# Kernel optimization log

Hardware: AMD Instinct MI355X
Metric: run time of the kernel (lower is better)

The kernel has to match this reference:

```python
import jax, jax.numpy as jnp
import numpy as np

NUM_EMBEDDINGS = 1024
EMBEDDING_DIM = 256
COMMITMENT_COST = 0.25
B, C, T = 16, 256, 4096


def setup_inputs() -> dict:
    key = jax.random.key(0)
    k_in, k_cb = jax.random.split(key)
    inputs = jax.random.normal(k_in, (B, C, T), dtype=jnp.float32)
    # matches nn.Embedding init uniform_(-1/K, 1/K)
    codebook = jax.random.uniform(
        k_cb, (NUM_EMBEDDINGS, EMBEDDING_DIM), dtype=jnp.float32,
        minval=-1.0 / NUM_EMBEDDINGS, maxval=1.0 / NUM_EMBEDDINGS)
    return {"inputs": inputs, "codebook": codebook}


def reference(inputs, codebook):
    # inputs: [B, C, T] -> [B, T, C] (channel-last), eval mode (no dead-code swap)
    x = jnp.transpose(inputs, (0, 2, 1))            # [B, T, C]
    flat = x.reshape(-1, EMBEDDING_DIM)             # [N, D]
    distances = (jnp.sum(flat * flat, axis=1, keepdims=True)
                 + jnp.sum(codebook * codebook, axis=1)
                 - 2.0 * jnp.matmul(flat, codebook.T))   # [N, K]
    encoding_indices = jnp.argmin(distances, axis=1)     # [N]
    quantized = codebook[encoding_indices].reshape(x.shape)  # [B, T, C]
    sg = jax.lax.stop_gradient
    e_latent_loss = jnp.mean(jnp.square(sg(quantized) - x))
    q_latent_loss = jnp.mean(jnp.square(quantized - sg(x)))
    vq_loss = e_latent_loss + COMMITMENT_COST * q_latent_loss
    quantized_st = x + sg(quantized - x)                 # straight-through
    quantized_st = jnp.transpose(quantized_st, (0, 2, 1))  # back to [B, C, T]
    indices = encoding_indices.reshape(B, T)
    return quantized_st, vq_loss, indices
```

## Files before the change

kernel.cpp:

```cpp
#include <hip/hip_runtime.h>
#include <stdint.h>

#define DIMS 256
#define NT 4096
#define NROWS 65536
#define THETA 1.5e-4f

typedef float    f32x4_t __attribute__((ext_vector_type(4)));
typedef _Float16 f16x8_t __attribute__((ext_vector_type(8)));
typedef _Float16 f16x4_t __attribute__((ext_vector_type(4)));

__global__ __launch_bounds__(64) void vq_prep(const float* __restrict__ cb,
                                              float* __restrict__ se,
                                              _Float16* __restrict__ cb16){
  __shared__ float sq[256];
  const int k = blockIdx.x;
  const int tid = threadIdx.x;
  float4 v = *(const float4*)(cb + (size_t)k*256 + tid*4);
  f16x4_t p;
  p.x = (_Float16)(v.x * 512.f);
  p.y = (_Float16)(v.y * 512.f);
  p.z = (_Float16)(v.z * 512.f);
  p.w = (_Float16)(v.w * 512.f);
  *(f16x4_t*)(cb16 + (size_t)k*256 + tid*4) = p;
  sq[tid*4+0] = __fmul_rn(v.x, v.x);
  sq[tid*4+1] = __fmul_rn(v.y, v.y);
  sq[tid*4+2] = __fmul_rn(v.z, v.z);
  sq[tid*4+3] = __fmul_rn(v.w, v.w);
  __syncthreads();
  if (tid < 16){
    const int h = tid >> 3, j = tid & 7;
    float r = sq[h*128 + j];
    #pragma unroll
    for (int i = 1; i < 16; ++i) r = __fadd_rn(r, sq[h*128 + j + 8*i]);
    r = __fadd_rn(r, __shfl_xor(r, 1));
    r = __fadd_rn(r, __shfl_xor(r, 2));
    r = __fadd_rn(r, __shfl_xor(r, 4));
    r = __fadd_rn(r, __shfl_xor(r, 8));
    if (tid == 0) se[k] = r;
  }
}


#define AH(r,c)    Ah[(size_t)(r)*264 + (c)]
#define BHL(s,k,c) Bh[((size_t)((s)*256 + (k)))*40 + (c)]
#define QQ(t,c)    q[(size_t)(t)*260 + (c)]

#define T2I(v, i, v1, i1, v2) { \
  bool lt = (v) < (v1); \
  (v2) = lt ? (v1) : fminf((v2), (v)); \
  (i1) = lt ? (i) : (i1); \
  (v1) = lt ? (v) : (v1); }

#define DECL_T2(M,R) \
  float b1_##M##R = 3.4e38f, b2_##M##R = 3.4e38f; int bi_##M##R = 0x7fffffff;

#define FOLD(M,R) { \
  float v; \
  v = fmaf(a##M##0[R], NEGI, ec0); T2I(v, kc0, b1_##M##R, bi_##M##R, b2_##M##R); \
  v = fmaf(a##M##1[R], NEGI, ec1); T2I(v, kc1, b1_##M##R, bi_##M##R, b2_##M##R); \
  v = fmaf(a##M##2[R], NEGI, ec2); T2I(v, kc2, b1_##M##R, bi_##M##R, b2_##M##R); \
  v = fmaf(a##M##3[R], NEGI, ec3); T2I(v, kc3, b1_##M##R, bi_##M##R, b2_##M##R); }

#define BSTEP(CC) { \
  *(f16x8_t*)&BHL((CC)&1, codeS, cOff)     = rb0; \
  *(f16x8_t*)&BHL((CC)&1, codeS, cOff + 8) = rb1; \
  if ((CC) < 7){ \
    const _Float16* p_ = bsrcKt + ((CC)+1)*32; \
    rb0 = *(const f16x8_t*)(p_); rb1 = *(const f16x8_t*)(p_ + 8); \
  } else if (kt < 3){ \
    const _Float16* p_ = bsrcKt + 256*DIMS; \
    rb0 = *(const f16x8_t*)(p_); rb1 = *(const f16x8_t*)(p_ + 8); \
  } \
  __syncthreads(); \
  { \
    f16x8_t bh0 = *(const f16x8_t*)&BHL((CC)&1, bC0, fq8); \
    f16x8_t bh1 = *(const f16x8_t*)&BHL((CC)&1, bC1, fq8); \
    f16x8_t bh2 = *(const f16x8_t*)&BHL((CC)&1, bC2, fq8); \
    f16x8_t bh3 = *(const f16x8_t*)&BHL((CC)&1, bC3, fq8); \
    f16x8_t ah0 = *(const f16x8_t*)&AH(wr32 + fr, (CC)*32 + fq8); \
    f16x8_t ah1 = *(const f16x8_t*)&AH(wr32 + 16 + fr, (CC)*32 + fq8); \
    a00 = __builtin_amdgcn_mfma_f32_16x16x32_f16(ah0, bh0, a00, 0, 0, 0); \
    a01 = __builtin_amdgcn_mfma_f32_16x16x32_f16(ah0, bh1, a01, 0, 0, 0); \
    a02 = __builtin_amdgcn_mfma_f32_16x16x32_f16(ah0, bh2, a02, 0, 0, 0); \
    a03 = __builtin_amdgcn_mfma_f32_16x16x32_f16(ah0, bh3, a03, 0, 0, 0); \
    a10 = __builtin_amdgcn_mfma_f32_16x16x32_f16(ah1, bh0, a10, 0, 0, 0); \
    a11 = __builtin_amdgcn_mfma_f32_16x16x32_f16(ah1, bh1, a11, 0, 0, 0); \
    a12 = __builtin_amdgcn_mfma_f32_16x16x32_f16(ah1, bh2, a12, 0, 0, 0); \
    a13 = __builtin_amdgcn_mfma_f32_16x16x32_f16(ah1, bh3, a13, 0, 0, 0); \
  } }

#define MSTEP(MK) { \
  float ov1 = __shfl_xor(v1, MK); int oi1 = __shfl_xor(i1, MK); float ov2 = __shfl_xor(v2, MK); \
  bool tk = ov1 < v1; \
  v2 = tk ? fminf(v1, ov2) : fminf(v2, ov1); \
  i1 = tk ? oi1 : i1; \
  v1 = tk ? ov1 : v1; }

#define MERGE(M,R) { \
  float v1 = b1_##M##R, v2 = b2_##M##R; int i1 = bi_##M##R; \
  MSTEP(1) MSTEP(2) MSTEP(4) MSTEP(8) \
  if (fr == 0) comb[(wr32 + (M)*16 + fq*4 + (R))*4 + wc] = make_float4(v1, __int_as_float(i1), v2, 0.f); }

__global__ __launch_bounds__(512, 1) void vq_scores(
    const float* __restrict__ x, const float* __restrict__ cb,
    const _Float16* __restrict__ cb16, const float* __restrict__ se,
    float* __restrict__ out0, float* __restrict__ out2,
    unsigned* __restrict__ wl, unsigned* __restrict__ cnt, double* __restrict__ accd)
{
  __shared__ __align__(16) char smem[79360];
  _Float16* Ah   = (_Float16*)smem;
  _Float16* Bh   = (_Float16*)(smem + 33792);
  float4*   comb = (float4*)(smem + 74752);
  int*      codeL= (int*)(smem + 78848);
  float*    sxa  = (float*)(smem + 79104);
  float*    q    = (float*)smem;

  const int tid  = threadIdx.x;
  const int lane = tid & 63;
  const int wid  = tid >> 6;
  const int wr   = wid >> 2;
  const int wc   = wid & 3;
  const int fr   = lane & 15;
  const int fq   = lane >> 4;
  const int wr32 = wr * 32;
  const int fq8  = fq * 8;
  const int n0   = blockIdx.x * 64;
  const int bb   = n0 >> 12;
  const int t0   = n0 & 4095;
  const float NEGI = -1.0f/256.0f;

  const int codeS = tid >> 1;
  const int cOff  = (tid & 1) << 4;

  f16x8_t rb0, rb1;
  {
    const _Float16* p_ = cb16 + (size_t)codeS * DIMS + cOff;
    rb0 = *(const f16x8_t*)(p_); rb1 = *(const f16x8_t*)(p_ + 8);
  }

  {
    const int dup = tid >> 7;
    const int c4  = tid & 7;
    const int tt  = ((tid >> 3) & 15) << 2;
    #pragma unroll
    for (int cc2 = 0; cc2 < 2; ++cc2){
      const int c0 = (dup*2 + cc2) * 32;
      const float* xp = x + ((size_t)(bb*DIMS + c0 + c4*4))*NT + t0 + tt;
      float4 va0 = *(const float4*)(xp);
      float4 va1 = *(const float4*)(xp + NT);
      float4 va2 = *(const float4*)(xp + 2*NT);
      float4 va3 = *(const float4*)(xp + 3*NT);
      #pragma unroll
      for (int j = 0; j < 4; ++j){
        f16x4_t p;
        p.x = (_Float16)((&va0.x)[j]);
        p.y = (_Float16)((&va1.x)[j]);
        p.z = (_Float16)((&va2.x)[j]);
        p.w = (_Float16)((&va3.x)[j]);
        *(f16x4_t*)&AH(tt + j, c0 + c4*4) = p;
      }
    }
  }

  const f32x4_t Z = {0.f, 0.f, 0.f, 0.f};
  f32x4_t a00=Z,a01=Z,a02=Z,a03=Z, a10=Z,a11=Z,a12=Z,a13=Z;
  DECL_T2(0,0) DECL_T2(0,1) DECL_T2(0,2) DECL_T2(0,3)
  DECL_T2(1,0) DECL_T2(1,1) DECL_T2(1,2) DECL_T2(1,3)

  const int bC0 = wc*64 + 0*16 + fr;
  const int bC1 = wc*64 + 1*16 + fr;
  const int bC2 = wc*64 + 2*16 + fr;
  const int bC3 = wc*64 + 3*16 + fr;

  for (int kt = 0; kt < 4; ++kt){
    const _Float16* bsrcKt = cb16 + ((size_t)(kt*256) + codeS) * DIMS + cOff;
    BSTEP(0) BSTEP(1) BSTEP(2) BSTEP(3)
    BSTEP(4) BSTEP(5) BSTEP(6) BSTEP(7)

    const int kb  = kt*256 + wc*64 + fr;
    const int kc0 = kb, kc1 = kb + 16, kc2 = kb + 32, kc3 = kb + 48;
    const float ec0 = se[kc0], ec1 = se[kc1], ec2 = se[kc2], ec3 = se[kc3];
    FOLD(0,0) FOLD(0,1) FOLD(0,2) FOLD(0,3)
    FOLD(1,0) FOLD(1,1) FOLD(1,2) FOLD(1,3)
    a00=Z;a01=Z;a02=Z;a03=Z; a10=Z;a11=Z;a12=Z;a13=Z;
  }

  MERGE(0,0) MERGE(0,1) MERGE(0,2) MERGE(0,3)
  MERGE(1,0) MERGE(1,1) MERGE(1,2) MERGE(1,3)
  __syncthreads();

  {
    const int row = tid >> 3, seg = tid & 7;
    float s = 0.f;
    #pragma unroll
    for (int k = 0; k < 4; ++k){
      f16x8_t hv = *(const f16x8_t*)&AH(row, seg*32 + k*8);
      #pragma unroll
      for (int e = 0; e < 8; ++e){
        float f = (float)hv[e];
        s = fmaf(f, f, s);
      }
    }
    s += __shfl_xor(s, 1);
    s += __shfl_xor(s, 2);
    s += __shfl_xor(s, 4);
    if (seg == 0) sxa[row] = s;
  }
  __syncthreads();

  if (tid < 64){
    float4 p = comb[tid*4 + 0];
    float v1 = p.x, v2 = p.z;
    int   i1 = __float_as_int(p.y);
    #pragma unroll
    for (int w = 1; w < 4; ++w){
      p = comb[tid*4 + w];
      bool tk = p.x < v1;
      v2 = tk ? fminf(v1, p.z) : fminf(v2, p.x);
      i1 = tk ? __float_as_int(p.y) : i1;
      v1 = tk ? p.x : v1;
    }
    const int r = n0 + tid;
    codeL[tid] = i1;
    out2[r] = (float)i1;
    bool flg = !(v2 - v1 >= THETA);
    if (flg){
      unsigned pos = atomicAdd(cnt, 1u);
      wl[pos] = (unsigned)r;
    }
    double c = flg ? 0.0 : (double)(sxa[tid] + v1);
    #pragma unroll
    for (int m = 1; m < 64; m <<= 1) c += __shfl_xor(c, m);
    if (tid == 0) atomicAdd(accd, c);
  }
  __syncthreads();

  {
    const int r = tid >> 3, seg = tid & 7;
    const float* src = cb + (size_t)codeL[r] * DIMS;
    #pragma unroll
    for (int k = 0; k < 8; ++k){
      float4 v = *(const float4*)(src + k*32 + seg*4);
      *(float4*)&QQ(r, k*32 + seg*4) = v;
    }
  }
  __syncthreads();

  {
    #pragma unroll
    for (int jj = 0; jj < 2; ++jj){
      const int c = wid*32 + jj*16 + (lane >> 2);
      float* dst = out0 + ((size_t)(bb*256 + c))*NT + t0;
      #pragma unroll
      for (int ii = 0; ii < 4; ++ii){
        const int tl = ii*16 + (lane & 3)*4;
        float4 v;
        v.x = QQ(tl + 0, c);
        v.y = QQ(tl + 1, c);
        v.z = QQ(tl + 2, c);
        v.w = QQ(tl + 3, c);
        *(float4*)(dst + tl) = v;
      }
    }
  }
}

__global__ __launch_bounds__(256) void vq_refine(
    const float* __restrict__ x, const float* __restrict__ cb,
    const float* __restrict__ se,
    const unsigned* __restrict__ wl, const unsigned* __restrict__ cnt,
    float* __restrict__ out2, float* __restrict__ out0, double* __restrict__ accd)
{
  __shared__ float eT[8][1024];
  __shared__ float xs[DIMS][8];
  __shared__ int   rows_s[8];
  __shared__ float sxs[8];
  __shared__ float wv[4][8];
  __shared__ int   wi[4][8];
  __shared__ int   wiF[8];

  const unsigned n = *cnt;
  const unsigned groups = (n + 7u) >> 3;
  const int tid  = threadIdx.x;
  const int lane = tid & 63;
  const int wid  = tid >> 6;

  for (unsigned g = blockIdx.x; g < groups; g += gridDim.x){
    __syncthreads();
    if (tid < 8){
      unsigned e = g*8u + (unsigned)tid;
      rows_s[tid] = (int)wl[e < n ? e : (n - 1u)];
    }
    __syncthreads();
    #pragma unroll
    for (int rep = 0; rep < 8; ++rep){
      int id = rep * 256 + tid;
      int c = id >> 3, r = id & 7;
      int row = rows_s[r];
      int b = row >> 12, t = row & 4095;
      xs[c][r] = x[((size_t)(b*DIMS + c))*NT + t];
    }
    __syncthreads();
    if (tid < 128){
      const int r = tid >> 4, hj = tid & 15;
      const int h = hj >> 3, j = hj & 7;
      float v0 = xs[h*128 + j][r];
      float s = __fmul_rn(v0, v0);
      #pragma unroll
      for (int i = 1; i < 16; ++i){
        float v = xs[h*128 + j + 8*i][r];
        s = __fadd_rn(s, __fmul_rn(v, v));
      }
      s = __fadd_rn(s, __shfl_xor(s, 1));
      s = __fadd_rn(s, __shfl_xor(s, 2));
      s = __fadd_rn(s, __shfl_xor(s, 4));
      s = __fadd_rn(s, __shfl_xor(s, 8));
      if (hj == 0) sxs[r] = s;
    }

    float s[8][4];
    #pragma unroll
    for (int r = 0; r < 8; ++r)
      #pragma unroll
      for (int u = 0; u < 4; ++u) s[r][u] = 0.f;

    for (int c0 = 0; c0 < DIMS; c0 += 8){
      __syncthreads();
      #pragma unroll
      for (int rep = 0; rep < 8; ++rep){
        int id2 = rep * 256 + tid;
        int k = id2 >> 1, qq = id2 & 1;
        float4 v = *(const float4*)&cb[(size_t)k * DIMS + c0 + qq * 4];
        eT[qq*4 + 0][k] = v.x; eT[qq*4 + 1][k] = v.y;
        eT[qq*4 + 2][k] = v.z; eT[qq*4 + 3][k] = v.w;
      }
      __syncthreads();
      #pragma unroll
      for (int cc = 0; cc < 8; ++cc){
        float4 ev = *(const float4*)&eT[cc][wid*256 + lane*4];
        #pragma unroll
        for (int r = 0; r < 8; ++r){
          float xv = xs[c0 + cc][r];
          s[r][0] = fmaf(xv, ev.x, s[r][0]);
          s[r][1] = fmaf(xv, ev.y, s[r][1]);
          s[r][2] = fmaf(xv, ev.z, s[r][2]);
          s[r][3] = fmaf(xv, ev.w, s[r][3]);
        }
      }
    }

    float4 sek = *(const float4*)&se[wid*256 + lane*4];
    #pragma unroll
    for (int r = 0; r < 8; ++r){
      const float sxv = sxs[r];
      float bv = 3.4e38f; int bi = 0x7fffffff;
      #pragma unroll
      for (int u = 0; u < 4; ++u){
        float d = __fsub_rn(__fadd_rn(sxv, (&sek.x)[u]),
                            __fadd_rn(s[r][u], s[r][u]));
        int k = wid*256 + lane*4 + u;
        if (d < bv || (d == bv && k < bi)) { bv = d; bi = k; }
      }
      #pragma unroll
      for (int m = 1; m < 64; m <<= 1){
        float ov = __shfl_xor(bv, m);
        int   oi = __shfl_xor(bi, m);
        if (ov < bv || (ov == bv && oi < bi)) { bv = ov; bi = oi; }
      }
      if (lane == 0){ wv[wid][r] = bv; wi[wid][r] = bi; }
    }
    __syncthreads();
    if (tid < 8){
      const int r = tid;
      float bv = wv[0][r]; int bi = wi[0][r];
      #pragma unroll
      for (int w = 1; w < 4; ++w){
        float ov = wv[w][r]; int oi = wi[w][r];
        if (ov < bv || (ov == bv && oi < bi)) { bv = ov; bi = oi; }
      }
      wiF[r] = bi;
      if (g*8u + (unsigned)r < n){
        int row = rows_s[r];
        out2[row] = (float)bi;
        atomicAdd(accd, (double)bv);
      }
    }
    __syncthreads();
    #pragma unroll
    for (int r = 0; r < 8; ++r){
      if (g*8u + (unsigned)r < n){
        int row  = rows_s[r];
        int code = wiF[r];
        out0[((size_t)((row >> 12)*256 + tid))*NT + (row & 4095)] = cb[(size_t)code*DIMS + tid];
      }
    }
  }
}

__global__ void vq_final(const double* __restrict__ accd, float* __restrict__ out1){
  *out1 = (float)(1.25 * (*accd) * (1.0 / 16777216.0));
}

extern "C" void kernel_launch(void* const* d_in, const int* in_sizes, int n_in,
                              void* d_out, int out_size, void* d_ws, size_t ws_size,
                              hipStream_t stream)
{
  const float* x  = (const float*)d_in[0];
  const float* cb = (const float*)d_in[1];
  float* out  = (float*)d_out;
  float* out0 = out;
  float* out1 = out + (size_t)16777216;
  float* out2 = out + (size_t)16777217;

  char* ws = (char*)d_ws;
  double*   accd = (double*)(ws + 0);
  unsigned* cnt  = (unsigned*)(ws + 8);
  float*    se   = (float*)(ws + 64);
  unsigned* wl   = (unsigned*)(ws + 4160);
  _Float16* cb16 = (_Float16*)(ws + 266304);

  hipMemsetAsync(d_ws, 0, 16, stream);
  vq_prep  <<<dim3(1024), dim3(64),  0, stream>>>(cb, se, cb16);
  vq_scores<<<dim3(1024), dim3(512), 0, stream>>>(x, cb, cb16, se, out0, out2, wl, cnt, accd);
  vq_refine<<<dim3(512),  dim3(256), 0, stream>>>(x, cb, se, wl, cnt, out2, out0, accd);
  vq_final <<<dim3(1),    dim3(1),   0, stream>>>(accd, out1);
}
```

Before: 172.2 us.

## Deepen codebook prefetch to two stages, hoist norms, batch refine rows by 16

In the main scoring kernel, codebook chunks are now prefetched two steps ahead using alternating register sets, and the global load is issued after the barrier instead of before it. The kt loop is fully unrolled and the codebook norms are loaded once into registers up front. The refine kernel now handles 16 candidate rows per group instead of 8, so each staged codebook tile is reused across twice as many rows. The cost is higher register pressure in both kernels, and the refine kernel needs more registers for its 16x4 accumulator array.

```diff
diff --git a/kernel.cpp b/kernel.cpp
--- a/kernel.cpp
+++ b/kernel.cpp
@@ -55,24 +55,24 @@
 #define DECL_T2(M,R) \
   float b1_##M##R = 3.4e38f, b2_##M##R = 3.4e38f; int bi_##M##R = 0x7fffffff;
 
-#define FOLD(M,R) { \
+#define FOLDK(KT,M,R) { \
   float v; \
-  v = fmaf(a##M##0[R], NEGI, ec0); T2I(v, kc0, b1_##M##R, bi_##M##R, b2_##M##R); \
-  v = fmaf(a##M##1[R], NEGI, ec1); T2I(v, kc1, b1_##M##R, bi_##M##R, b2_##M##R); \
-  v = fmaf(a##M##2[R], NEGI, ec2); T2I(v, kc2, b1_##M##R, bi_##M##R, b2_##M##R); \
-  v = fmaf(a##M##3[R], NEGI, ec3); T2I(v, kc3, b1_##M##R, bi_##M##R, b2_##M##R); }
-
-#define BSTEP(CC) { \
-  *(f16x8_t*)&BHL((CC)&1, codeS, cOff)     = rb0; \
-  *(f16x8_t*)&BHL((CC)&1, codeS, cOff + 8) = rb1; \
-  if ((CC) < 7){ \
-    const _Float16* p_ = bsrcKt + ((CC)+1)*32; \
-    rb0 = *(const f16x8_t*)(p_); rb1 = *(const f16x8_t*)(p_ + 8); \
-  } else if (kt < 3){ \
-    const _Float16* p_ = bsrcKt + 256*DIMS; \
-    rb0 = *(const f16x8_t*)(p_); rb1 = *(const f16x8_t*)(p_ + 8); \
+  v = fmaf(a##M##0[R], NEGI, seh[(KT)*4+0]); T2I(v, (KT)*256 + wcfr +  0, b1_##M##R, bi_##M##R, b2_##M##R); \
+  v = fmaf(a##M##1[R], NEGI, seh[(KT)*4+1]); T2I(v, (KT)*256 + wcfr + 16, b1_##M##R, bi_##M##R, b2_##M##R); \
+  v = fmaf(a##M##2[R], NEGI, seh[(KT)*4+2]); T2I(v, (KT)*256 + wcfr + 32, b1_##M##R, bi_##M##R, b2_##M##R); \
+  v = fmaf(a##M##3[R], NEGI, seh[(KT)*4+3]); T2I(v, (KT)*256 + wcfr + 48, b1_##M##R, bi_##M##R, b2_##M##R); }
+
+#define BSTEP(KT, CC, S) { \
+  *(f16x8_t*)&BHL((CC)&1, codeS, cOff)     = rb##S##0; \
+  *(f16x8_t*)&BHL((CC)&1, codeS, cOff + 8) = rb##S##1; \
+  __syncthreads(); \
+  { \
+    const int nn = (KT)*8 + (CC) + 2; \
+    if (nn < 32){ \
+      const _Float16* p_ = cb16 + ((size_t)((nn>>3)*256) + codeS)*DIMS + (nn&7)*32 + cOff; \
+      rb##S##0 = *(const f16x8_t*)(p_); rb##S##1 = *(const f16x8_t*)(p_ + 8); \
+    } \
   } \
-  __syncthreads(); \
   { \
     f16x8_t bh0 = *(const f16x8_t*)&BHL((CC)&1, bC0, fq8); \
     f16x8_t bh1 = *(const f16x8_t*)&BHL((CC)&1, bC1, fq8); \
@@ -90,6 +90,13 @@
     a13 = __builtin_amdgcn_mfma_f32_16x16x32_f16(ah1, bh3, a13, 0, 0, 0); \
   } }
 
+#define KTSTEP(KT) { \
+  BSTEP(KT,0,A) BSTEP(KT,1,B) BSTEP(KT,2,A) BSTEP(KT,3,B) \
+  BSTEP(KT,4,A) BSTEP(KT,5,B) BSTEP(KT,6,A) BSTEP(KT,7,B) \
+  FOLDK(KT,0,0) FOLDK(KT,0,1) FOLDK(KT,0,2) FOLDK(KT,0,3) \
+  FOLDK(KT,1,0) FOLDK(KT,1,1) FOLDK(KT,1,2) FOLDK(KT,1,3) \
+  a00=Z;a01=Z;a02=Z;a03=Z; a10=Z;a11=Z;a12=Z;a13=Z; }
+
 #define MSTEP(MK) { \
   float ov1 = __shfl_xor(v1, MK); int oi1 = __shfl_xor(i1, MK); float ov2 = __shfl_xor(v2, MK); \
   bool tk = ov1 < v1; \
@@ -125,6 +132,7 @@
   const int fq   = lane >> 4;
   const int wr32 = wr * 32;
   const int fq8  = fq * 8;
+  const int wcfr = wc*64 + fr;
   const int n0   = blockIdx.x * 64;
   const int bb   = n0 >> 12;
   const int t0   = n0 & 4095;
@@ -133,10 +141,19 @@
   const int codeS = tid >> 1;
   const int cOff  = (tid & 1) << 4;
 
-  f16x8_t rb0, rb1;
+  float seh[16];
+  #pragma unroll
+  for (int qq = 0; qq < 16; ++qq)
+    seh[qq] = se[(qq>>2)*256 + wcfr + (qq&3)*16];
+
+  f16x8_t rbA0, rbA1, rbB0, rbB1;
   {
     const _Float16* p_ = cb16 + (size_t)codeS * DIMS + cOff;
-    rb0 = *(const f16x8_t*)(p_); rb1 = *(const f16x8_t*)(p_ + 8);
+    rbA0 = *(const f16x8_t*)(p_); rbA1 = *(const f16x8_t*)(p_ + 8);
+  }
+  {
+    const _Float16* p_ = cb16 + (size_t)codeS * DIMS + 32 + cOff;
+    rbB0 = *(const f16x8_t*)(p_); rbB1 = *(const f16x8_t*)(p_ + 8);
   }
 
   {
@@ -173,18 +190,7 @@
   const int bC2 = wc*64 + 2*16 + fr;
   const int bC3 = wc*64 + 3*16 + fr;
 
-  for (int kt = 0; kt < 4; ++kt){
-    const _Float16* bsrcKt = cb16 + ((size_t)(kt*256) + codeS) * DIMS + cOff;
-    BSTEP(0) BSTEP(1) BSTEP(2) BSTEP(3)
-    BSTEP(4) BSTEP(5) BSTEP(6) BSTEP(7)
-
-    const int kb  = kt*256 + wc*64 + fr;
-    const int kc0 = kb, kc1 = kb + 16, kc2 = kb + 32, kc3 = kb + 48;
-    const float ec0 = se[kc0], ec1 = se[kc1], ec2 = se[kc2], ec3 = se[kc3];
-    FOLD(0,0) FOLD(0,1) FOLD(0,2) FOLD(0,3)
-    FOLD(1,0) FOLD(1,1) FOLD(1,2) FOLD(1,3)
-    a00=Z;a01=Z;a02=Z;a03=Z; a10=Z;a11=Z;a12=Z;a13=Z;
-  }
+  KTSTEP(0) KTSTEP(1) KTSTEP(2) KTSTEP(3)
 
   MERGE(0,0) MERGE(0,1) MERGE(0,2) MERGE(0,3)
   MERGE(1,0) MERGE(1,1) MERGE(1,2) MERGE(1,3)
@@ -273,36 +279,35 @@
     float* __restrict__ out2, float* __restrict__ out0, double* __restrict__ accd)
 {
   __shared__ float eT[8][1024];
-  __shared__ float xs[DIMS][8];
-  __shared__ int   rows_s[8];
-  __shared__ float sxs[8];
-  __shared__ float wv[4][8];
-  __shared__ int   wi[4][8];
-  __shared__ int   wiF[8];
+  __shared__ float xs[DIMS][16];
+  __shared__ int   rows_s[16];
+  __shared__ float sxs[16];
+  __shared__ float wv[4][16];
+  __shared__ int   wi[4][16];
+  __shared__ int   wiF[16];
 
   const unsigned n = *cnt;
-  const unsigned groups = (n + 7u) >> 3;
+  const unsigned groups = (n + 15u) >> 4;
   const int tid  = threadIdx.x;
   const int lane = tid & 63;
   const int wid  = tid >> 6;
 
   for (unsigned g = blockIdx.x; g < groups; g += gridDim.x){
     __syncthreads();
-    if (tid < 8){
-      unsigned e = g*8u + (unsigned)tid;
+    if (tid < 16){
+      unsigned e = g*16u + (unsigned)tid;
       rows_s[tid] = (int)wl[e < n ? e : (n - 1u)];
     }
     __syncthreads();
     #pragma unroll
-    for (int rep = 0; rep < 8; ++rep){
+    for (int rep = 0; rep < 16; ++rep){
       int id = rep * 256 + tid;
-      int c = id >> 3, r = id & 7;
+      int c = id >> 4, r = id & 15;
       int row = rows_s[r];
-      int b = row >> 12, t = row & 4095;
-      xs[c][r] = x[((size_t)(b*DIMS + c))*NT + t];
+      xs[c][r] = x[((size_t)((row >> 12)*DIMS + c))*NT + (row & 4095)];
     }
     __syncthreads();
-    if (tid < 128){
+    {
       const int r = tid >> 4, hj = tid & 15;
       const int h = hj >> 3, j = hj & 7;
       float v0 = xs[h*128 + j][r];
@@ -319,9 +324,9 @@
       if (hj == 0) sxs[r] = s;
     }
 
-    float s[8][4];
-    #pragma unroll
-    for (int r = 0; r < 8; ++r)
+    float s[16][4];
+    #pragma unroll
+    for (int r = 0; r < 16; ++r)
       #pragma unroll
       for (int u = 0; u < 4; ++u) s[r][u] = 0.f;
 
@@ -340,7 +345,7 @@
       for (int cc = 0; cc < 8; ++cc){
         float4 ev = *(const float4*)&eT[cc][wid*256 + lane*4];
         #pragma unroll
-        for (int r = 0; r < 8; ++r){
+        for (int r = 0; r < 16; ++r){
           float xv = xs[c0 + cc][r];
           s[r][0] = fmaf(xv, ev.x, s[r][0]);
           s[r][1] = fmaf(xv, ev.y, s[r][1]);
@@ -352,7 +357,7 @@
 
     float4 sek = *(const float4*)&se[wid*256 + lane*4];
     #pragma unroll
-    for (int r = 0; r < 8; ++r){
+    for (int r = 0; r < 16; ++r){
       const float sxv = sxs[r];
       float bv = 3.4e38f; int bi = 0x7fffffff;
       #pragma unroll
@@ -371,7 +376,7 @@
       if (lane == 0){ wv[wid][r] = bv; wi[wid][r] = bi; }
     }
     __syncthreads();
-    if (tid < 8){
+    if (tid < 16){
       const int r = tid;
       float bv = wv[0][r]; int bi = wi[0][r];
       #pragma unroll
@@ -380,7 +385,7 @@
         if (ov < bv || (ov == bv && oi < bi)) { bv = ov; bi = oi; }
       }
       wiF[r] = bi;
-      if (g*8u + (unsigned)r < n){
+      if (g*16u + (unsigned)r < n){
         int row = rows_s[r];
         out2[row] = (float)bi;
         atomicAdd(accd, (double)bv);
@@ -388,8 +393,8 @@
     }
     __syncthreads();
     #pragma unroll
-    for (int r = 0; r < 8; ++r){
-      if (g*8u + (unsigned)r < n){
+    for (int r = 0; r < 16; ++r){
+      if (g*16u + (unsigned)r < n){
         int row  = rows_s[r];
         int code = wiF[r];
         out0[((size_t)((row >> 12)*256 + tid))*NT + (row & 4095)] = cb[(size_t)code*DIMS + tid];
```

Measured after the change: 201.2 us. +16.9%, slower.
